# Kernel optimization log

Measured on AMD Instinct MI355X. Metric: run time of the kernel, lower is better.

## Reference

```python
import jax, jax.numpy as jnp
import numpy as np

B, D_IN, NQ, D_OUT = 65536, 1024, 64, 1024
PI = float(np.pi)


def setup_inputs() -> dict:
    key = jax.random.key(0)
    ks = jax.random.split(key, 6)
    return {
        "x": jax.random.normal(ks[0], (B, D_IN), dtype=jnp.float32),
        "W_in": jax.random.normal(ks[1], (NQ, D_IN), dtype=jnp.float32) * 0.02,
        "b_in": jax.random.normal(ks[2], (NQ,), dtype=jnp.float32) * 0.02,
        "quantum_params": jax.random.normal(ks[3], (NQ, 3), dtype=jnp.float32) * 0.1,
        "W_out": jax.random.normal(ks[4], (D_OUT, NQ), dtype=jnp.float32) * 0.02,
        "b_out": jax.random.normal(ks[5], (D_OUT,), dtype=jnp.float32) * 0.02,
    }


def reference(x, W_in, b_in, quantum_params, W_out, b_out):
    # input linear + tanh: [B, NQ]
    h = jnp.tanh(x @ W_in.T + b_in)
    # quantum forward, vectorized over (batch, qubit):
    # state = cos(h*pi/2)*cos(p0) + sin(p1)*cos(p2)
    angles = h * PI
    p0, p1, p2 = quantum_params[:, 0], quantum_params[:, 1], quantum_params[:, 2]
    state = jnp.cos(angles * 0.5) * jnp.cos(p0) + jnp.sin(p1) * jnp.cos(p2)
    # output linear: [B, D_OUT]
    return state @ W_out.T + b_out
```

## Files before the change

### kernel.cpp

```cpp
#include <hip/hip_runtime.h>
#include <hip/hip_bf16.h>
#include <math.h>

#define NB 65536
#define DIN 1024
#define NQ 64
#define DOUT 1024

typedef __attribute__((ext_vector_type(8))) short bf16x8;
typedef __attribute__((ext_vector_type(4))) float f32x4;
typedef unsigned short u16;

__device__ __forceinline__ u16 f2bf(float f) {
    union { float f; unsigned u; } v; v.f = f;
    return (u16)((v.u + 0x7fffu + ((v.u >> 16) & 1u)) >> 16);
}

__global__ __launch_bounds__(256) void kP(const float* __restrict__ W_in,
                                          const float* __restrict__ W_out,
                                          const float* __restrict__ qp,
                                          u16* __restrict__ Wbf,
                                          u16* __restrict__ Wobf,
                                          float* __restrict__ cp0,
                                          float* __restrict__ cq) {
    int tid = blockIdx.x * 256 + threadIdx.x;
    {
        int j = tid & 7, l = (tid >> 3) & 63, n = (tid >> 9) & 3, c = tid >> 11;
        int row = n * 16 + (l & 15);
        int k   = c * 32 + (l >> 4) * 8 + j;
        Wbf[tid] = f2bf(W_in[row * DIN + k]);
    }
    {
        int j = tid & 7, l = (tid >> 3) & 63, kf = (tid >> 9) & 1, n = tid >> 10;
        int col = n * 16 + (l & 15);
        int k   = kf * 32 + (l >> 4) * 8 + j;
        Wobf[tid] = f2bf(W_out[col * NQ + k]);
    }
    if (tid < NQ) {
        cp0[tid] = cosf(qp[tid * 3 + 0]);
        cq[tid]  = sinf(qp[tid * 3 + 1]) * cosf(qp[tid * 3 + 2]);
    }
}

__global__ __launch_bounds__(256, 4) void kF(const float* __restrict__ x,
                                             const u16* __restrict__ Wbf,
                                             const float* __restrict__ b_in,
                                             const float* __restrict__ cp0,
                                             const float* __restrict__ cq,
                                             const u16* __restrict__ Wobf,
                                             const float* __restrict__ b_out,
                                             float* __restrict__ out) {
    __shared__ u16   st[4][16][72];
    __shared__ float boutL[DOUT];
    __shared__ float binL[NQ], cp0L[NQ], cqL[NQ];

    const int tid = threadIdx.x;
    const int w = tid >> 6, l = tid & 63;
    const int r = l & 15, kg = l >> 4;
    const int row0 = blockIdx.x * 64;

    *(float4*)(boutL + tid * 4) = *(const float4*)(b_out + tid * 4);
    if (tid < NQ) { binL[tid] = b_in[tid]; cp0L[tid] = cp0[tid]; cqL[tid] = cq[tid]; }
    __syncthreads();

    const char* xS   = (const char*)x + (size_t)row0 * DIN * 4;
    const char* outS = (const char*)out + (size_t)row0 * DOUT * 4;
    const unsigned voff_x   = (unsigned)(w * 16 + r) * (DIN * 4) + kg * 32;
    const unsigned voff_l16 = (unsigned)l * 16;
    unsigned vo[4];
    #pragma unroll
    for (int i = 0; i < 4; i++)
        vo[i] = (unsigned)(w * 16 + kg * 4 + i) * (DOUT * 4) + r * 4;

#define LDX(slot, t) { \
    asm volatile("global_load_dwordx4 %0, %1, %2 offset:%3" \
        : "=v"(xr[slot][0]) : "v"(voff_x), "s"(xS), "i"((t) * 128)); \
    asm volatile("global_load_dwordx4 %0, %1, %2 offset:%3" \
        : "=v"(xr[slot][1]) : "v"(voff_x), "s"(xS), "i"((t) * 128 + 16)); }
#define LDW(slot, t) { const char* wS_ = (const char*)Wbf + (t) * 4096; \
    asm volatile("global_load_dwordx4 %0, %1, %2 offset:0"    : "=v"(wbr[slot][0]) : "v"(voff_l16), "s"(wS_)); \
    asm volatile("global_load_dwordx4 %0, %1, %2 offset:1024" : "=v"(wbr[slot][1]) : "v"(voff_l16), "s"(wS_)); \
    asm volatile("global_load_dwordx4 %0, %1, %2 offset:2048" : "=v"(wbr[slot][2]) : "v"(voff_l16), "s"(wS_)); \
    asm volatile("global_load_dwordx4 %0, %1, %2 offset:3072" : "=v"(wbr[slot][3]) : "v"(voff_l16), "s"(wS_)); }
#define PBLOAD(slot, g) { const char* oS_ = (const char*)Wobf + (g) * 4096; \
    asm volatile("global_load_dwordx4 %0, %1, %2 offset:0"    : "=v"(wob[slot][0][0]) : "v"(voff_l16), "s"(oS_)); \
    asm volatile("global_load_dwordx4 %0, %1, %2 offset:1024" : "=v"(wob[slot][0][1]) : "v"(voff_l16), "s"(oS_)); \
    asm volatile("global_load_dwordx4 %0, %1, %2 offset:2048" : "=v"(wob[slot][1][0]) : "v"(voff_l16), "s"(oS_)); \
    asm volatile("global_load_dwordx4 %0, %1, %2 offset:3072" : "=v"(wob[slot][1][1]) : "v"(voff_l16), "s"(oS_)); }

    f32x4 acc[4] = {f32x4{0,0,0,0}, f32x4{0,0,0,0}, f32x4{0,0,0,0}, f32x4{0,0,0,0}};
    float4 xr[3][2];
    bf16x8 wbr[3][4];

    LDX(0, 0) LDW(0, 0)
    LDX(1, 1) LDW(1, 1)

    #pragma unroll
    for (int t = 0; t < 32; ++t) {
        const int s = t % 3, s2 = (t + 2) % 3;
        if (t + 2 < 32) { LDX(s2, t + 2) LDW(s2, t + 2) }
        __builtin_amdgcn_sched_barrier(0);
        if (t < 30)       asm volatile("s_waitcnt vmcnt(12)" ::: "memory");
        else if (t == 30) asm volatile("s_waitcnt vmcnt(6)"  ::: "memory");
        else              asm volatile("s_waitcnt vmcnt(0)"  ::: "memory");
        __builtin_amdgcn_sched_barrier(0);
        union { bf16x8 v; unsigned u[4]; } a;
        asm("v_cvt_pk_bf16_f32 %0, %1, %2" : "=v"(a.u[0]) : "v"(xr[s][0].x), "v"(xr[s][0].y));
        asm("v_cvt_pk_bf16_f32 %0, %1, %2" : "=v"(a.u[1]) : "v"(xr[s][0].z), "v"(xr[s][0].w));
        asm("v_cvt_pk_bf16_f32 %0, %1, %2" : "=v"(a.u[2]) : "v"(xr[s][1].x), "v"(xr[s][1].y));
        asm("v_cvt_pk_bf16_f32 %0, %1, %2" : "=v"(a.u[3]) : "v"(xr[s][1].z), "v"(xr[s][1].w));
        #pragma unroll
        for (int n = 0; n < 4; ++n)
            acc[n] = __builtin_amdgcn_mfma_f32_16x16x32_bf16(a.v, wbr[s][n], acc[n], 0, 0, 0);
    }

    bf16x8 wob[3][2][2];
    PBLOAD(0, 0) PBLOAD(1, 1)
    __builtin_amdgcn_sched_barrier(0);

    #pragma unroll
    for (int n = 0; n < 4; ++n) {
        int q = n * 16 + r;
        float bi = binL[q], c0q = cp0L[q], c1q = cqL[q];
        #pragma unroll
        for (int i = 0; i < 4; ++i) {
            float av = acc[n][i] + bi;
            float e2 = __builtin_amdgcn_exp2f(av * 2.8853900817779268f);
            float th = 1.0f - 2.0f * __builtin_amdgcn_rcpf(e2 + 1.0f);
            float sv = __builtin_amdgcn_cosf(th * 0.25f) * c0q + c1q;
            st[w][kg * 4 + i][q] = f2bf(sv);
        }
    }
    bf16x8 sa0 = *(const bf16x8*)&st[w][r][kg * 8];
    bf16x8 sa1 = *(const bf16x8*)&st[w][r][32 + kg * 8];

    #pragma unroll
    for (int g = 0; g < 32; ++g) {
        const int s = g % 3, s2 = (g + 2) % 3;
        if (g + 2 < 32) { PBLOAD(s2, g + 2) }
        __builtin_amdgcn_sched_barrier(0);
        if (g == 0)       asm volatile("s_waitcnt vmcnt(8)"  ::: "memory");
        else if (g == 1)  asm volatile("s_waitcnt vmcnt(16)" ::: "memory");
        else if (g < 30)  asm volatile("s_waitcnt vmcnt(24)" ::: "memory");
        else if (g == 30) asm volatile("s_waitcnt vmcnt(20)" ::: "memory");
        else              asm volatile("s_waitcnt vmcnt(16)" ::: "memory");
        __builtin_amdgcn_sched_barrier(0);
        #pragma unroll
        for (int ti = 0; ti < 2; ++ti) {
            const int tile = g * 2 + ti;
            f32x4 a2 = {0.0f, 0.0f, 0.0f, 0.0f};
            a2 = __builtin_amdgcn_mfma_f32_16x16x32_bf16(sa0, wob[s][ti][0], a2, 0, 0, 0);
            a2 = __builtin_amdgcn_mfma_f32_16x16x32_bf16(sa1, wob[s][ti][1], a2, 0, 0, 0);
            float bo = boutL[tile * 16 + r];
            #pragma unroll
            for (int i = 0; i < 4; ++i) {
                float d = a2[i] + bo;
                asm volatile("global_store_dword %0, %1, %2 offset:%3"
                             :: "v"(vo[i]), "v"(d), "s"(outS), "i"(tile * 64) : "memory");
            }
        }
    }
#undef LDX
#undef LDW
#undef PBLOAD
}

extern "C" void kernel_launch(void* const* d_in, const int* in_sizes, int n_in,
                              void* d_out, int out_size, void* d_ws, size_t ws_size,
                              hipStream_t stream) {
    const float* x    = (const float*)d_in[0];
    const float* W_in = (const float*)d_in[1];
    const float* b_in = (const float*)d_in[2];
    const float* qp   = (const float*)d_in[3];
    const float* W_out= (const float*)d_in[4];
    const float* b_out= (const float*)d_in[5];
    float* out = (float*)d_out;

    char* ws = (char*)d_ws;
    u16*   Wbf  = (u16*)(ws);
    u16*   Wobf = (u16*)(ws + 131072);
    float* cp0  = (float*)(ws + 262144);
    float* cq   = (float*)(ws + 262400);

    kP<<<256, 256, 0, stream>>>(W_in, W_out, qp, Wbf, Wobf, cp0, cq);
    kF<<<NB / 64, 256, 0, stream>>>(x, Wbf, b_in, cp0, cq, Wobf, b_out, out);
}
```

Measured before the change: 171.5 us.

## Stage operands through LDS with global_load_lds in single-wave blocks

After: 158.1 us. 7.8% less time.

```diff
diff --git a/kernel.cpp b/kernel.cpp
--- a/kernel.cpp
+++ b/kernel.cpp
@@ -14,6 +14,17 @@
 __device__ __forceinline__ u16 f2bf(float f) {
     union { float f; unsigned u; } v; v.f = f;
     return (u16)((v.u + 0x7fffu + ((v.u >> 16) & 1u)) >> 16);
+}
+
+__device__ __forceinline__ void gll16(const void* g, void* l) {
+    __builtin_amdgcn_global_load_lds(
+        (const __attribute__((address_space(1))) unsigned int*)g,
+        (__attribute__((address_space(3))) unsigned int*)l, 16, 0, 0);
+}
+__device__ __forceinline__ void gll4(const void* g, void* l) {
+    __builtin_amdgcn_global_load_lds(
+        (const __attribute__((address_space(1))) unsigned int*)g,
+        (__attribute__((address_space(3))) unsigned int*)l, 4, 0, 0);
 }
 
 __global__ __launch_bounds__(256) void kP(const float* __restrict__ W_in,
@@ -42,81 +53,82 @@
     }
 }
 
-__global__ __launch_bounds__(256, 4) void kF(const float* __restrict__ x,
-                                             const u16* __restrict__ Wbf,
-                                             const float* __restrict__ b_in,
-                                             const float* __restrict__ cp0,
-                                             const float* __restrict__ cq,
-                                             const u16* __restrict__ Wobf,
-                                             const float* __restrict__ b_out,
-                                             float* __restrict__ out) {
-    __shared__ u16   st[4][16][72];
-    __shared__ float boutL[DOUT];
-    __shared__ float binL[NQ], cp0L[NQ], cqL[NQ];
-
-    const int tid = threadIdx.x;
-    const int w = tid >> 6, l = tid & 63;
+__global__ __launch_bounds__(64) void kF(const float* __restrict__ x,
+                                         const u16* __restrict__ Wbf,
+                                         const float* __restrict__ b_in,
+                                         const float* __restrict__ cp0,
+                                         const float* __restrict__ cq,
+                                         const u16* __restrict__ Wobf,
+                                         const float* __restrict__ b_out,
+                                         float* __restrict__ out) {
+    __shared__ __align__(16) char  ring[3 * 6144];
+    __shared__ __align__(16) u16   st[16][72];
+    __shared__ __align__(16) float boutL[DOUT];
+    __shared__ __align__(16) float binL[NQ], cp0L[NQ], cqL[NQ];
+
+    const int l = threadIdx.x;
     const int r = l & 15, kg = l >> 4;
-    const int row0 = blockIdx.x * 64;
-
-    *(float4*)(boutL + tid * 4) = *(const float4*)(b_out + tid * 4);
-    if (tid < NQ) { binL[tid] = b_in[tid]; cp0L[tid] = cp0[tid]; cqL[tid] = cq[tid]; }
-    __syncthreads();
-
-    const char* xS   = (const char*)x + (size_t)row0 * DIN * 4;
-    const char* outS = (const char*)out + (size_t)row0 * DOUT * 4;
-    const unsigned voff_x   = (unsigned)(w * 16 + r) * (DIN * 4) + kg * 32;
-    const unsigned voff_l16 = (unsigned)l * 16;
-    unsigned vo[4];
-    #pragma unroll
-    for (int i = 0; i < 4; i++)
-        vo[i] = (unsigned)(w * 16 + kg * 4 + i) * (DOUT * 4) + r * 4;
-
-#define LDX(slot, t) { \
-    asm volatile("global_load_dwordx4 %0, %1, %2 offset:%3" \
-        : "=v"(xr[slot][0]) : "v"(voff_x), "s"(xS), "i"((t) * 128)); \
-    asm volatile("global_load_dwordx4 %0, %1, %2 offset:%3" \
-        : "=v"(xr[slot][1]) : "v"(voff_x), "s"(xS), "i"((t) * 128 + 16)); }
-#define LDW(slot, t) { const char* wS_ = (const char*)Wbf + (t) * 4096; \
-    asm volatile("global_load_dwordx4 %0, %1, %2 offset:0"    : "=v"(wbr[slot][0]) : "v"(voff_l16), "s"(wS_)); \
-    asm volatile("global_load_dwordx4 %0, %1, %2 offset:1024" : "=v"(wbr[slot][1]) : "v"(voff_l16), "s"(wS_)); \
-    asm volatile("global_load_dwordx4 %0, %1, %2 offset:2048" : "=v"(wbr[slot][2]) : "v"(voff_l16), "s"(wS_)); \
-    asm volatile("global_load_dwordx4 %0, %1, %2 offset:3072" : "=v"(wbr[slot][3]) : "v"(voff_l16), "s"(wS_)); }
-#define PBLOAD(slot, g) { const char* oS_ = (const char*)Wobf + (g) * 4096; \
-    asm volatile("global_load_dwordx4 %0, %1, %2 offset:0"    : "=v"(wob[slot][0][0]) : "v"(voff_l16), "s"(oS_)); \
-    asm volatile("global_load_dwordx4 %0, %1, %2 offset:1024" : "=v"(wob[slot][0][1]) : "v"(voff_l16), "s"(oS_)); \
-    asm volatile("global_load_dwordx4 %0, %1, %2 offset:2048" : "=v"(wob[slot][1][0]) : "v"(voff_l16), "s"(oS_)); \
-    asm volatile("global_load_dwordx4 %0, %1, %2 offset:3072" : "=v"(wob[slot][1][1]) : "v"(voff_l16), "s"(oS_)); }
+    const int row0 = blockIdx.x * 16;
+
+    gll4(b_in + l, binL);
+    gll4(cp0 + l, cp0L);
+    gll4(cq  + l, cqL);
+    gll16(b_out + l * 4 +   0, (char*)boutL);
+    gll16(b_out + l * 4 + 256, (char*)boutL + 1024);
+    gll16(b_out + l * 4 + 512, (char*)boutL + 2048);
+    gll16(b_out + l * 4 + 768, (char*)boutL + 3072);
+
+    const char* xs1 = (const char*)x + (size_t)(row0 + (l >> 3)) * (DIN * 4)
+                                     + (size_t)((((l & 7) ^ (l >> 3))) * 16);
+    const char* xs2 = xs1 + (size_t)8 * DIN * 4;
+    const char* wsrc = (const char*)Wbf  + l * 16;
+    const char* osrc = (const char*)Wobf + l * 16;
+
+#define STAGE_A(t) { char* buf_ = ring + ((t) % 3) * 6144; \
+    gll16(xs1 + (size_t)(t) * 128, buf_); \
+    gll16(xs2 + (size_t)(t) * 128, buf_ + 1024); \
+    const char* ws_ = wsrc + (size_t)(t) * 4096; \
+    gll16(ws_,        buf_ + 2048); \
+    gll16(ws_ + 1024, buf_ + 3072); \
+    gll16(ws_ + 2048, buf_ + 4096); \
+    gll16(ws_ + 3072, buf_ + 5120); }
+
+#define STAGE_B(g) { char* ob_ = ring + ((g) % 3) * 4096; \
+    const char* os_ = osrc + (size_t)(g) * 4096; \
+    gll16(os_,        ob_); \
+    gll16(os_ + 1024, ob_ + 1024); \
+    gll16(os_ + 2048, ob_ + 2048); \
+    gll16(os_ + 3072, ob_ + 3072); }
+
+    STAGE_A(0) STAGE_A(1)
 
     f32x4 acc[4] = {f32x4{0,0,0,0}, f32x4{0,0,0,0}, f32x4{0,0,0,0}, f32x4{0,0,0,0}};
-    float4 xr[3][2];
-    bf16x8 wbr[3][4];
-
-    LDX(0, 0) LDW(0, 0)
-    LDX(1, 1) LDW(1, 1)
+    const int sA = (2 * kg) ^ (r & 7);
+    const int sB = sA ^ 1;
 
     #pragma unroll
     for (int t = 0; t < 32; ++t) {
-        const int s = t % 3, s2 = (t + 2) % 3;
-        if (t + 2 < 32) { LDX(s2, t + 2) LDW(s2, t + 2) }
-        __builtin_amdgcn_sched_barrier(0);
-        if (t < 30)       asm volatile("s_waitcnt vmcnt(12)" ::: "memory");
+        if (t <= 29) STAGE_A(t + 2)
+        if (t <= 29)      asm volatile("s_waitcnt vmcnt(12)" ::: "memory");
         else if (t == 30) asm volatile("s_waitcnt vmcnt(6)"  ::: "memory");
         else              asm volatile("s_waitcnt vmcnt(0)"  ::: "memory");
-        __builtin_amdgcn_sched_barrier(0);
+        const char* buf = ring + (t % 3) * 6144;
+        const char* xrow = buf + (r >> 3) * 1024 + (r & 7) * 128;
+        float4 xa = *(const float4*)(xrow + sA * 16);
+        float4 xb = *(const float4*)(xrow + sB * 16);
         union { bf16x8 v; unsigned u[4]; } a;
-        asm("v_cvt_pk_bf16_f32 %0, %1, %2" : "=v"(a.u[0]) : "v"(xr[s][0].x), "v"(xr[s][0].y));
-        asm("v_cvt_pk_bf16_f32 %0, %1, %2" : "=v"(a.u[1]) : "v"(xr[s][0].z), "v"(xr[s][0].w));
-        asm("v_cvt_pk_bf16_f32 %0, %1, %2" : "=v"(a.u[2]) : "v"(xr[s][1].x), "v"(xr[s][1].y));
-        asm("v_cvt_pk_bf16_f32 %0, %1, %2" : "=v"(a.u[3]) : "v"(xr[s][1].z), "v"(xr[s][1].w));
+        asm("v_cvt_pk_bf16_f32 %0, %1, %2" : "=v"(a.u[0]) : "v"(xa.x), "v"(xa.y));
+        asm("v_cvt_pk_bf16_f32 %0, %1, %2" : "=v"(a.u[1]) : "v"(xa.z), "v"(xa.w));
+        asm("v_cvt_pk_bf16_f32 %0, %1, %2" : "=v"(a.u[2]) : "v"(xb.x), "v"(xb.y));
+        asm("v_cvt_pk_bf16_f32 %0, %1, %2" : "=v"(a.u[3]) : "v"(xb.z), "v"(xb.w));
         #pragma unroll
-        for (int n = 0; n < 4; ++n)
-            acc[n] = __builtin_amdgcn_mfma_f32_16x16x32_bf16(a.v, wbr[s][n], acc[n], 0, 0, 0);
-    }
-
-    bf16x8 wob[3][2][2];
-    PBLOAD(0, 0) PBLOAD(1, 1)
-    __builtin_amdgcn_sched_barrier(0);
+        for (int n = 0; n < 4; ++n) {
+            bf16x8 b = *(const bf16x8*)(buf + 2048 + n * 1024 + l * 16);
+            acc[n] = __builtin_amdgcn_mfma_f32_16x16x32_bf16(a.v, b, acc[n], 0, 0, 0);
+        }
+    }
+
+    STAGE_B(0) STAGE_B(1)
 
     #pragma unroll
     for (int n = 0; n < 4; ++n) {
@@ -128,29 +140,35 @@
             float e2 = __builtin_amdgcn_exp2f(av * 2.8853900817779268f);
             float th = 1.0f - 2.0f * __builtin_amdgcn_rcpf(e2 + 1.0f);
             float sv = __builtin_amdgcn_cosf(th * 0.25f) * c0q + c1q;
-            st[w][kg * 4 + i][q] = f2bf(sv);
+            st[kg * 4 + i][q] = f2bf(sv);
         }
     }
-    bf16x8 sa0 = *(const bf16x8*)&st[w][r][kg * 8];
-    bf16x8 sa1 = *(const bf16x8*)&st[w][r][32 + kg * 8];
+    bf16x8 sa0 = *(const bf16x8*)&st[r][kg * 8];
+    bf16x8 sa1 = *(const bf16x8*)&st[r][32 + kg * 8];
+
+    const char* outS = (const char*)out + (size_t)row0 * DOUT * 4;
+    unsigned vo[4];
+    #pragma unroll
+    for (int i = 0; i < 4; ++i)
+        vo[i] = (unsigned)(kg * 4 + i) * (DOUT * 4) + r * 4;
 
     #pragma unroll
     for (int g = 0; g < 32; ++g) {
-        const int s = g % 3, s2 = (g + 2) % 3;
-        if (g + 2 < 32) { PBLOAD(s2, g + 2) }
-        __builtin_amdgcn_sched_barrier(0);
+        if (g <= 29) STAGE_B(g + 2)
         if (g == 0)       asm volatile("s_waitcnt vmcnt(8)"  ::: "memory");
         else if (g == 1)  asm volatile("s_waitcnt vmcnt(16)" ::: "memory");
-        else if (g < 30)  asm volatile("s_waitcnt vmcnt(24)" ::: "memory");
+        else if (g <= 29) asm volatile("s_waitcnt vmcnt(24)" ::: "memory");
         else if (g == 30) asm volatile("s_waitcnt vmcnt(20)" ::: "memory");
         else              asm volatile("s_waitcnt vmcnt(16)" ::: "memory");
-        __builtin_amdgcn_sched_barrier(0);
+        const char* ob = ring + (g % 3) * 4096;
         #pragma unroll
         for (int ti = 0; ti < 2; ++ti) {
             const int tile = g * 2 + ti;
+            bf16x8 b0 = *(const bf16x8*)(ob + ti * 2048 + l * 16);
+            bf16x8 b1 = *(const bf16x8*)(ob + ti * 2048 + 1024 + l * 16);
             f32x4 a2 = {0.0f, 0.0f, 0.0f, 0.0f};
-            a2 = __builtin_amdgcn_mfma_f32_16x16x32_bf16(sa0, wob[s][ti][0], a2, 0, 0, 0);
-            a2 = __builtin_amdgcn_mfma_f32_16x16x32_bf16(sa1, wob[s][ti][1], a2, 0, 0, 0);
+            a2 = __builtin_amdgcn_mfma_f32_16x16x32_bf16(sa0, b0, a2, 0, 0, 0);
+            a2 = __builtin_amdgcn_mfma_f32_16x16x32_bf16(sa1, b1, a2, 0, 0, 0);
             float bo = boutL[tile * 16 + r];
             #pragma unroll
             for (int i = 0; i < 4; ++i) {
@@ -160,9 +178,8 @@
             }
         }
     }
-#undef LDX
-#undef LDW
-#undef PBLOAD
+#undef STAGE_A
+#undef STAGE_B
 }
 
 extern "C" void kernel_launch(void* const* d_in, const int* in_sizes, int n_in,
@@ -183,5 +200,5 @@
     float* cq   = (float*)(ws + 262400);
 
     kP<<<256, 256, 0, stream>>>(W_in, W_out, qp, Wbf, Wobf, cp0, cq);
-    kF<<<NB / 64, 256, 0, stream>>>(x, Wbf, b_in, cp0, cq, Wobf, b_out, out);
-}
+    kF<<<NB / 16, 64, 0, stream>>>(x, Wbf, b_in, cp0, cq, Wobf, b_out, out);
+}
```
